# Optimization experiments

Measured on AMD Instinct MI355X. Metric: run time of the kernel, lower is better.

## Reference

```python
import jax, jax.numpy as jnp
import numpy as np

B, T, D, O = 8, 128, 512, 512


def setup_inputs() -> dict:
    key = jax.random.key(0)
    ks = jax.random.split(key, 10)
    w = 0.02  # small init scale, mimics GlorotNormal magnitude
    return {
        "inputs": jax.random.normal(ks[0], (B, T, D), dtype=jnp.float32),
        "Wa": jax.random.normal(ks[1], (O, O), dtype=jnp.float32) * w,
        "Ua": jax.random.normal(ks[2], (D, O), dtype=jnp.float32) * w,
        "Va": jax.random.normal(ks[3], (O, 1), dtype=jnp.float32) * w,
        "Ba": jax.random.normal(ks[4], (1, O), dtype=jnp.float32) * w,
        "Wo": jax.random.normal(ks[5], (O, 1), dtype=jnp.float32) * w,
        "Uo": jax.random.normal(ks[6], (D, O), dtype=jnp.float32) * w,
        "Co": jax.random.normal(ks[7], (D, O), dtype=jnp.float32) * w,
        "Bo": jax.random.normal(ks[8], (1, O), dtype=jnp.float32) * w,
        "emb": jax.random.normal(ks[9], (O, O), dtype=jnp.float32) * w,
    }


def reference(inputs, Wa, Ua, Va, Ba, Wo, Uo, Co, Bo, emb):
    # inputs: [B,T,D]. Precompute loop-invariant attention keys (incl. Ba).
    UaH = jnp.einsum('btd,do->bto', inputs, Ua) + Ba  # [B,T,O]
    # GRU 'prev_state' arg at step t is inputs[:, t-1, :] (t=0 -> last step).
    prev_h = jnp.roll(inputs, 1, axis=1)              # [B,T,D]
    xs = jnp.swapaxes(prev_h, 0, 1)                   # [T,B,D]
    b, o = inputs.shape[0], Wa.shape[0]

    def step(prev_pred, h_prev):
        # --- attention cell (query = sigmoid(prev_pred)) ---
        s = jax.nn.sigmoid(prev_pred)                  # [B,O]
        WaS = s @ Wa                                   # [B,O]
        e = jnp.tanh(UaH + WaS[:, None, :])            # [B,T,O]
        scores = jnp.squeeze(e @ Va, -1)               # [B,T]
        sm = jax.nn.softmax(scores, axis=1)            # softmax over timesteps
        ctx = jnp.einsum('bt,btd->bd', sm, inputs)     # [B,D]
        # --- cascaded GRU cell ---
        emb_out = jax.nn.softmax(prev_pred, axis=-1) @ emb  # [B,O]
        WoY = emb_out @ Wo                             # [B,1] (broadcasts over O)
        pred = WoY + h_prev @ Uo + ctx @ Co + Bo       # [B,O]
        return pred, pred

    init = jnp.zeros((b, o), dtype=inputs.dtype)
    _, out = jax.lax.scan(step, init, xs)              # [T,B,O]
    return jnp.swapaxes(out, 0, 1)                     # [B,T,O]
```

## Files before the change

kernel.cpp:

```cpp
#include <hip/hip_runtime.h>

#define L2E 1.44269504088896340736f


typedef unsigned long long ull;

__device__ __forceinline__ void st_pack(ull* p, float v, int tag) {
  ull u = (((ull)(unsigned)tag) << 32) | (ull)__float_as_uint(v);
  __hip_atomic_store(p, u, __ATOMIC_RELAXED, __HIP_MEMORY_SCOPE_AGENT);
}
__device__ __forceinline__ ull ld_pack(const ull* p) {
  return __hip_atomic_load(p, __ATOMIC_RELAXED, __HIP_MEMORY_SCOPE_AGENT);
}

__global__ __launch_bounds__(256) void gemm_pre(
    const float* __restrict__ A, const float* __restrict__ Ua,
    const float* __restrict__ Uo, const float* __restrict__ Co,
    float* __restrict__ XW)
{
  __shared__ float sA[64][33];
  __shared__ float sB[32][68];
  const int r0 = blockIdx.x * 64;
  const int c0 = blockIdx.y * 64;
  const float* Wm; int cc0;
  if (c0 < 512)       { Wm = Ua; cc0 = c0; }
  else if (c0 < 1024) { Wm = Uo; cc0 = c0 - 512; }
  else                { Wm = Co; cc0 = c0 - 1024; }
  const int tid = threadIdx.x;
  const int ty4 = (tid >> 4) * 4;
  const int tx4 = (tid & 15) * 4;
  float acc[4][4] = {};
  for (int k0 = 0; k0 < 512; k0 += 32) {
    for (int t4 = tid; t4 < 512; t4 += 256) {
      int row = t4 >> 3, kq = (t4 & 7) << 2;
      float4 v = *reinterpret_cast<const float4*>(&A[(size_t)(r0 + row) * 512 + k0 + kq]);
      sA[row][kq] = v.x; sA[row][kq + 1] = v.y; sA[row][kq + 2] = v.z; sA[row][kq + 3] = v.w;
    }
    for (int t4 = tid; t4 < 512; t4 += 256) {
      int kk = t4 >> 4, cq = (t4 & 15) << 2;
      float4 v = *reinterpret_cast<const float4*>(&Wm[(size_t)(k0 + kk) * 512 + cc0 + cq]);
      sB[kk][cq] = v.x; sB[kk][cq + 1] = v.y; sB[kk][cq + 2] = v.z; sB[kk][cq + 3] = v.w;
    }
    __syncthreads();
    #pragma unroll 8
    for (int kk = 0; kk < 32; ++kk) {
      float a0 = sA[ty4 + 0][kk], a1 = sA[ty4 + 1][kk];
      float a2 = sA[ty4 + 2][kk], a3 = sA[ty4 + 3][kk];
      float4 bv = *reinterpret_cast<const float4*>(&sB[kk][tx4]);
      acc[0][0] += a0 * bv.x; acc[0][1] += a0 * bv.y; acc[0][2] += a0 * bv.z; acc[0][3] += a0 * bv.w;
      acc[1][0] += a1 * bv.x; acc[1][1] += a1 * bv.y; acc[1][2] += a1 * bv.z; acc[1][3] += a1 * bv.w;
      acc[2][0] += a2 * bv.x; acc[2][1] += a2 * bv.y; acc[2][2] += a2 * bv.z; acc[2][3] += a2 * bv.w;
      acc[3][0] += a3 * bv.x; acc[3][1] += a3 * bv.y; acc[3][2] += a3 * bv.z; acc[3][3] += a3 * bv.w;
    }
    __syncthreads();
  }
  for (int i = 0; i < 4; ++i) {
    float4 v = make_float4(acc[i][0], acc[i][1], acc[i][2], acc[i][3]);
    *reinterpret_cast<float4*>(&XW[(size_t)(r0 + ty4 + i) * 1536 + c0 + tx4]) = v;
  }
}

__global__ __launch_bounds__(512) void embwo_kernel(
    const float* __restrict__ emb, const float* __restrict__ Wo,
    float* __restrict__ gEmbWo)
{
  const int lane = threadIdx.x & 63;
  const int wv = threadIdx.x >> 6;
  const int kbase = blockIdx.x * 64 + wv * 8;
  for (int i = 0; i < 8; ++i) {
    const int k = kbase + i;
    float acc = 0.f;
    #pragma unroll
    for (int c = 0; c < 8; ++c) {
      int o = lane + 64 * c;
      acc += emb[(size_t)k * 512 + o] * Wo[o];
    }
    #pragma unroll
    for (int d = 1; d < 64; d <<= 1) acc += __shfl_xor(acc, d);
    if (lane == 0) gEmbWo[k] = acc;
  }
}

__global__ __launch_bounds__(256) void coop_scan(
    const float* __restrict__ Wa, const float* __restrict__ Va,
    const float* __restrict__ Ba, const float* __restrict__ Bo,
    const float* __restrict__ gXW, const float* __restrict__ gEmbWo,
    ull* slotP64, ull* slotS64, float* __restrict__ out)
{
  extern __shared__ float smem[];
  float* sWa   = smem;
  float* sUaHT = smem + 16384;
  float* sICo  = smem + 20512;
  float* sP1   = smem + 24608;
  float* sPred = smem + 28704;
  float* sS    = smem + 29216;
  float* sEmb  = smem + 29728;
  float* sVa   = smem + 30240;
  float* sWaS  = smem + 30272;
  float* sSm   = smem + 30304;
  float* sRedB = smem + 30432;
  float* sRed  = smem + 30688;

  const int tid = threadIdx.x;
  const int lane = tid & 63;
  const int wv = tid >> 6;
  const int b = blockIdx.x & 7;
  const int j = blockIdx.x >> 3;
  const int obase = j * 32;

  for (int idx = tid; idx < 512 * 32; idx += 256) {
    int k = idx >> 5, oo = idx & 31;
    sWa[idx] = Wa[(size_t)k * 512 + obase + oo];
  }
  for (int idx = tid; idx < 128 * 32; idx += 256) {
    int tt = idx >> 5, oo = idx & 31;
    int col = obase + oo;
    const float* rowp = gXW + (size_t)(b * 128 + tt) * 1536;
    sUaHT[oo * 129 + tt] = rowp[col] + Ba[col];
    sICo[tt * 32 + oo] = rowp[1024 + col];
    int tprev = (tt + 127) & 127;
    sP1[tt * 32 + oo] = gXW[(size_t)(b * 128 + tprev) * 1536 + 512 + col] + Bo[col];
  }
  if (tid < 32) sVa[tid] = Va[obase + tid];
  sEmb[tid] = gEmbWo[tid]; sEmb[tid + 256] = gEmbWo[tid + 256];
  sPred[tid] = 0.f; sPred[tid + 256] = 0.f;

  for (int t = 0; t < 128; ++t) {
    __syncthreads();

    float p1 = sPred[tid], p2 = sPred[tid + 256];
    sS[tid]       = 1.f / (1.f + exp2f(-p1 * L2E));
    sS[tid + 256] = 1.f / (1.f + exp2f(-p2 * L2E));
    float e1 = exp2f(p1 * L2E), e2 = exp2f(p2 * L2E);
    float Ep = e1 + e2;
    float Dp = e1 * sEmb[tid] + e2 * sEmb[tid + 256];
    #pragma unroll
    for (int d = 1; d < 64; d <<= 1) { Ep += __shfl_xor(Ep, d); Dp += __shfl_xor(Dp, d); }
    if (lane == 0) { sRed[wv] = Ep; sRed[4 + wv] = Dp; }
    __syncthreads();
    const float WoY = (sRed[4] + sRed[5] + sRed[6] + sRed[7])
                    / (sRed[0] + sRed[1] + sRed[2] + sRed[3]);

    {
      const int o = tid & 31, kg = tid >> 5, kb = kg * 64;
      float acc = 0.f;
      #pragma unroll 16
      for (int i = 0; i < 64; ++i) acc += sS[kb + i] * sWa[(kb + i) * 32 + o];
      sRedB[kg * 32 + o] = acc;
    }
    __syncthreads();
    if (tid < 32) {
      float w = 0.f;
      #pragma unroll
      for (int g = 0; g < 8; ++g) w += sRedB[g * 32 + tid];
      sWaS[tid] = w;
    }
    __syncthreads();

    {
      const int h = tid & 1, tp = tid >> 1;
      float acc = 0.f;
      #pragma unroll
      for (int i = 0; i < 16; ++i) {
        const int oo = h * 16 + i;
        float u = sUaHT[oo * 129 + tp] + sWaS[oo];
        float ex = exp2f(u * (2.f * L2E));
        acc += (1.f - 2.f / (1.f + ex)) * sVa[oo];
      }
      acc += __shfl_xor(acc, 1);
      if (h == 0)
        st_pack(slotS64 + (((t & 1) * 8 + b) * 16 + j) * 128 + tp, acc, t + 1);
    }

    if (tid < 128) {
      const ull* basep = slotS64 + ((t & 1) * 8 + b) * 2048 + tid;
      const unsigned want = (unsigned)(t + 1);
      float sc = 0.f;
      unsigned mask = 0xFFFFu;
      while (mask) {
        #pragma unroll
        for (int jj = 0; jj < 16; ++jj) {
          if (mask & (1u << jj)) {
            ull v = ld_pack(basep + jj * 128);
            if ((unsigned)(v >> 32) == want) {
              sc += __uint_as_float((unsigned)v);
              mask &= ~(1u << jj);
            }
          }
        }
      }
      float ev = exp2f(sc * L2E);
      sSm[tid] = ev;
      float sv = ev;
      #pragma unroll
      for (int d = 1; d < 64; d <<= 1) sv += __shfl_xor(sv, d);
      if (lane == 0) sRed[8 + wv] = sv;
    }
    __syncthreads();
    const float rden = 1.f / (sRed[8] + sRed[9]);

    {
      const int o = tid & 31, g = tid >> 5, tb = g * 16;
      float acc = 0.f;
      #pragma unroll
      for (int i = 0; i < 16; ++i) acc += sSm[tb + i] * sICo[(tb + i) * 32 + o];
      sRedB[g * 32 + o] = acc;
    }
    __syncthreads();
    if (tid < 32) {
      float c = 0.f;
      #pragma unroll
      for (int g2 = 0; g2 < 8; ++g2) c += sRedB[g2 * 32 + tid];
      float pr = WoY + sP1[t * 32 + tid] + c * rden;
      out[(size_t)(b * 128 + t) * 512 + obase + tid] = pr;
      if (t < 127)
        st_pack(slotP64 + ((t & 1) * 8 + b) * 512 + obase + tid, pr, t + 1);
    }

    if (t < 127) {
      const ull* pp = slotP64 + ((t & 1) * 8 + b) * 512;
      const unsigned want = (unsigned)(t + 1);
      ull v0, v1; bool d0 = false, d1 = false;
      do {
        if (!d0) { v0 = ld_pack(pp + tid);       d0 = ((unsigned)(v0 >> 32) == want); }
        if (!d1) { v1 = ld_pack(pp + tid + 256); d1 = ((unsigned)(v1 >> 32) == want); }
      } while (!(d0 && d1));
      sPred[tid]       = __uint_as_float((unsigned)v0);
      sPred[tid + 256] = __uint_as_float((unsigned)v1);
    }
  }
}

extern "C" void kernel_launch(void* const* d_in, const int* in_sizes, int n_in,
                              void* d_out, int out_size, void* d_ws, size_t ws_size,
                              hipStream_t stream)
{
  const float* inputs = (const float*)d_in[0];
  const float* Wa  = (const float*)d_in[1];
  const float* Ua  = (const float*)d_in[2];
  const float* Va  = (const float*)d_in[3];
  const float* Ba  = (const float*)d_in[4];
  const float* Wo  = (const float*)d_in[5];
  const float* Uo  = (const float*)d_in[6];
  const float* Co  = (const float*)d_in[7];
  const float* Bo  = (const float*)d_in[8];
  const float* emb = (const float*)d_in[9];
  float* out = (float*)d_out;

  char* ws = (char*)d_ws;
  ull*   slotP64 = (ull*)(ws + 16384);
  ull*   slotS64 = (ull*)(ws + 81920);
  float* gEmbWo  = (float*)(ws + 344064);
  float* gXW     = (float*)(ws + 360448);


  dim3 gg(16, 24);
  gemm_pre<<<gg, 256, 0, stream>>>(inputs, Ua, Uo, Co, gXW);
  embwo_kernel<<<8, 512, 0, stream>>>(emb, Wo, gEmbWo);

  const int smem_bytes = 30704 * 4;
  hipFuncSetAttribute((const void*)coop_scan,
                      hipFuncAttributeMaxDynamicSharedMemorySize, smem_bytes);
  coop_scan<<<128, 256, smem_bytes, stream>>>(Wa, Va, Ba, Bo, gXW, gEmbWo,
                                              slotP64, slotS64, out);
}
```

Measured before the change: 1.189 ms.

## Compute full pred redundantly per block to drop cross-block pred exchange

Each block of a batch now computes all 512 prediction outputs itself, reading the inputs@Co projection from global memory stored as packed bf16. This removes the second cross-block spin-wait per step, where predictions were exchanged through tagged global slots. The cost is 16x redundant context-GEMV work, which adds global and L2 traffic of about 128 KB per block per step. Storing the projection in bf16 also lowers precision relative to the fp32 reference.

```diff
diff --git a/kernel.cpp b/kernel.cpp
--- a/kernel.cpp
+++ b/kernel.cpp
@@ -12,11 +12,15 @@
 __device__ __forceinline__ ull ld_pack(const ull* p) {
   return __hip_atomic_load(p, __ATOMIC_RELAXED, __HIP_MEMORY_SCOPE_AGENT);
 }
+__device__ __forceinline__ unsigned bf16rne(float x) {
+  unsigned u = __float_as_uint(x);
+  return (u + 0x7FFFu + ((u >> 16) & 1u)) >> 16;
+}
 
 __global__ __launch_bounds__(256) void gemm_pre(
     const float* __restrict__ A, const float* __restrict__ Ua,
     const float* __restrict__ Uo, const float* __restrict__ Co,
-    float* __restrict__ XW)
+    float* __restrict__ XW, unsigned* __restrict__ ICoB)
 {
   __shared__ float sA[64][33];
   __shared__ float sB[32][68];
@@ -54,9 +58,20 @@
     }
     __syncthreads();
   }
-  for (int i = 0; i < 4; ++i) {
-    float4 v = make_float4(acc[i][0], acc[i][1], acc[i][2], acc[i][3]);
-    *reinterpret_cast<float4*>(&XW[(size_t)(r0 + ty4 + i) * 1536 + c0 + tx4]) = v;
+  if (c0 < 1024) {
+    for (int i = 0; i < 4; ++i) {
+      float4 v = make_float4(acc[i][0], acc[i][1], acc[i][2], acc[i][3]);
+      *reinterpret_cast<float4*>(&XW[(size_t)(r0 + ty4 + i) * 1024 + c0 + tx4]) = v;
+    }
+  } else {
+    const int ob = c0 - 1024 + tx4;
+    for (int i = 0; i < 4; ++i) {
+      int row = r0 + ty4 + i;
+      unsigned w0 = bf16rne(acc[i][0]) | (bf16rne(acc[i][1]) << 16);
+      unsigned w1 = bf16rne(acc[i][2]) | (bf16rne(acc[i][3]) << 16);
+      uint2 w = make_uint2(w0, w1);
+      *reinterpret_cast<uint2*>(&ICoB[(size_t)row * 256 + (ob >> 1)]) = w;
+    }
   }
 }
 
@@ -84,22 +99,22 @@
 __global__ __launch_bounds__(256) void coop_scan(
     const float* __restrict__ Wa, const float* __restrict__ Va,
     const float* __restrict__ Ba, const float* __restrict__ Bo,
-    const float* __restrict__ gXW, const float* __restrict__ gEmbWo,
-    ull* slotP64, ull* slotS64, float* __restrict__ out)
+    const float* __restrict__ gXW, const unsigned* __restrict__ gICoB,
+    const float* __restrict__ gEmbWo, ull* slotS64, float* __restrict__ out)
 {
   extern __shared__ float smem[];
-  float* sWa   = smem;
-  float* sUaHT = smem + 16384;
-  float* sICo  = smem + 20512;
-  float* sP1   = smem + 24608;
-  float* sPred = smem + 28704;
-  float* sS    = smem + 29216;
-  float* sEmb  = smem + 29728;
-  float* sVa   = smem + 30240;
-  float* sWaS  = smem + 30272;
-  float* sSm   = smem + 30304;
-  float* sRedB = smem + 30432;
-  float* sRed  = smem + 30688;
+  float* sWa    = smem;
+  float* sUaHT  = smem + 16384;
+  float* sPred  = smem + 20512;
+  float* sS     = smem + 21024;
+  float* sEmb   = smem + 21536;
+  float* sBo    = smem + 22048;
+  float* sP1row = smem + 22560;
+  float* sSm    = smem + 23072;
+  float* sRedB  = smem + 23200;
+  float* sRed   = smem + 23456;
+  float* sVa    = smem + 23472;
+  float* sWaS   = smem + 23504;
 
   const int tid = threadIdx.x;
   const int lane = tid & 63;
@@ -107,6 +122,7 @@
   const int b = blockIdx.x & 7;
   const int j = blockIdx.x >> 3;
   const int obase = j * 32;
+  const int u = tid;
 
   for (int idx = tid; idx < 512 * 32; idx += 256) {
     int k = idx >> 5, oo = idx & 31;
@@ -115,15 +131,14 @@
   for (int idx = tid; idx < 128 * 32; idx += 256) {
     int tt = idx >> 5, oo = idx & 31;
     int col = obase + oo;
-    const float* rowp = gXW + (size_t)(b * 128 + tt) * 1536;
-    sUaHT[oo * 129 + tt] = rowp[col] + Ba[col];
-    sICo[tt * 32 + oo] = rowp[1024 + col];
-    int tprev = (tt + 127) & 127;
-    sP1[tt * 32 + oo] = gXW[(size_t)(b * 128 + tprev) * 1536 + 512 + col] + Bo[col];
+    sUaHT[oo * 129 + tt] = gXW[(size_t)(b * 128 + tt) * 1024 + col] + Ba[col];
   }
   if (tid < 32) sVa[tid] = Va[obase + tid];
-  sEmb[tid] = gEmbWo[tid]; sEmb[tid + 256] = gEmbWo[tid + 256];
-  sPred[tid] = 0.f; sPred[tid + 256] = 0.f;
+  sEmb[tid] = gEmbWo[tid];       sEmb[tid + 256] = gEmbWo[tid + 256];
+  sBo[tid]  = Bo[tid];           sBo[tid + 256]  = Bo[tid + 256];
+  sPred[tid] = 0.f;              sPred[tid + 256] = 0.f;
+
+  const unsigned* myICo = gICoB + (size_t)b * 32768;
 
   for (int t = 0; t < 128; ++t) {
     __syncthreads();
@@ -131,6 +146,12 @@
     float p1 = sPred[tid], p2 = sPred[tid + 256];
     sS[tid]       = 1.f / (1.f + exp2f(-p1 * L2E));
     sS[tid + 256] = 1.f / (1.f + exp2f(-p2 * L2E));
+    {
+      const int tprev = (t + 127) & 127;
+      const float* uorow = gXW + (size_t)(b * 128 + tprev) * 1024 + 512;
+      sP1row[tid]       = uorow[tid] + sBo[tid];
+      sP1row[tid + 256] = uorow[tid + 256] + sBo[tid + 256];
+    }
     float e1 = exp2f(p1 * L2E), e2 = exp2f(p2 * L2E);
     float Ep = e1 + e2;
     float Dp = e1 * sEmb[tid] + e2 * sEmb[tid + 256];
@@ -163,8 +184,8 @@
       #pragma unroll
       for (int i = 0; i < 16; ++i) {
         const int oo = h * 16 + i;
-        float u = sUaHT[oo * 129 + tp] + sWaS[oo];
-        float ex = exp2f(u * (2.f * L2E));
+        float uu = sUaHT[oo * 129 + tp] + sWaS[oo];
+        float ex = exp2f(uu * (2.f * L2E));
         acc += (1.f - 2.f / (1.f + ex)) * sVa[oo];
       }
       acc += __shfl_xor(acc, 1);
@@ -200,33 +221,23 @@
     const float rden = 1.f / (sRed[8] + sRed[9]);
 
     {
-      const int o = tid & 31, g = tid >> 5, tb = g * 16;
-      float acc = 0.f;
-      #pragma unroll
-      for (int i = 0; i < 16; ++i) acc += sSm[tb + i] * sICo[(tb + i) * 32 + o];
-      sRedB[g * 32 + o] = acc;
-    }
-    __syncthreads();
-    if (tid < 32) {
-      float c = 0.f;
-      #pragma unroll
-      for (int g2 = 0; g2 < 8; ++g2) c += sRedB[g2 * 32 + tid];
-      float pr = WoY + sP1[t * 32 + tid] + c * rden;
-      out[(size_t)(b * 128 + t) * 512 + obase + tid] = pr;
-      if (t < 127)
-        st_pack(slotP64 + ((t & 1) * 8 + b) * 512 + obase + tid, pr, t + 1);
-    }
-
-    if (t < 127) {
-      const ull* pp = slotP64 + ((t & 1) * 8 + b) * 512;
-      const unsigned want = (unsigned)(t + 1);
-      ull v0, v1; bool d0 = false, d1 = false;
-      do {
-        if (!d0) { v0 = ld_pack(pp + tid);       d0 = ((unsigned)(v0 >> 32) == want); }
-        if (!d1) { v1 = ld_pack(pp + tid + 256); d1 = ((unsigned)(v1 >> 32) == want); }
-      } while (!(d0 && d1));
-      sPred[tid]       = __uint_as_float((unsigned)v0);
-      sPred[tid + 256] = __uint_as_float((unsigned)v1);
+      float a0 = 0.f, a1 = 0.f;
+      const unsigned* col = myICo + u;
+      #pragma unroll 8
+      for (int tt = 0; tt < 128; ++tt) {
+        float s = sSm[tt];
+        unsigned w = col[(size_t)tt * 256];
+        a0 = fmaf(s, __uint_as_float(w << 16), a0);
+        a1 = fmaf(s, __uint_as_float(w & 0xFFFF0000u), a1);
+      }
+      float pred0 = WoY + sP1row[2 * u]     + a0 * rden;
+      float pred1 = WoY + sP1row[2 * u + 1] + a1 * rden;
+      sPred[2 * u]     = pred0;
+      sPred[2 * u + 1] = pred1;
+      if (u >= (obase >> 1) && u < (obase >> 1) + 16) {
+        *reinterpret_cast<float2*>(&out[((size_t)(b * 128 + t)) * 512 + 2 * u]) =
+            make_float2(pred0, pred1);
+      }
     }
   }
 }
@@ -248,19 +259,18 @@
   float* out = (float*)d_out;
 
   char* ws = (char*)d_ws;
-  ull*   slotP64 = (ull*)(ws + 16384);
-  ull*   slotS64 = (ull*)(ws + 81920);
-  float* gEmbWo  = (float*)(ws + 344064);
-  float* gXW     = (float*)(ws + 360448);
-
+  ull*      slotS64 = (ull*)(ws + 0);
+  float*    gEmbWo  = (float*)(ws + 262144);
+  unsigned* gICoB   = (unsigned*)(ws + 264192);
+  float*    gXW     = (float*)(ws + 1313792);
 
   dim3 gg(16, 24);
-  gemm_pre<<<gg, 256, 0, stream>>>(inputs, Ua, Uo, Co, gXW);
+  gemm_pre<<<gg, 256, 0, stream>>>(inputs, Ua, Uo, Co, gXW, gICoB);
   embwo_kernel<<<8, 512, 0, stream>>>(emb, Wo, gEmbWo);
 
-  const int smem_bytes = 30704 * 4;
+  const int smem_bytes = 23536 * 4;
   hipFuncSetAttribute((const void*)coop_scan,
                       hipFuncAttributeMaxDynamicSharedMemorySize, smem_bytes);
-  coop_scan<<<128, 256, smem_bytes, stream>>>(Wa, Va, Ba, Bo, gXW, gEmbWo,
-                                              slotP64, slotS64, out);
-}
+  coop_scan<<<128, 256, smem_bytes, stream>>>(Wa, Va, Ba, Bo, gXW, gICoB,
+                                              gEmbWo, slotS64, out);
+}
```

After: 1.365 ms. 14.8% more time.
